# Optimization experiments

Measured on AMD Instinct MI355X. Metric: run time of the kernel, lower is better.

Reference implementation:

```python
import jax, jax.numpy as jnp
import numpy as np

B, D, H = 65536, 3, 256  # collocation batch, coord dim, hidden width


def setup_inputs() -> dict:
    key = jax.random.key(0)
    ks = jax.random.split(key, 8)

    def init(k, shape, fan_in):
        return jax.random.normal(k, shape, dtype=jnp.float32) * np.float32(1.0 / np.sqrt(fan_in))

    return {
        "x": jax.random.uniform(ks[0], (B, D), dtype=jnp.float32, minval=0.1, maxval=1.0),
        "W0": init(ks[1], (D, H), D), "b0": jnp.zeros((H,), jnp.float32),
        "W1": init(ks[2], (H, H), H), "b1": jnp.zeros((H,), jnp.float32),
        "W2": init(ks[3], (H, H), H), "b2": jnp.zeros((H,), jnp.float32),
        "W3": init(ks[4], (H, H), H), "b3": jnp.zeros((H,), jnp.float32),
        "Wout": init(ks[5], (H, 1), H), "bout": jnp.zeros((1,), jnp.float32),
    }


def reference(x, W0, b0, W1, b1, W2, b2, W3, b3, Wout, bout):
    # Scalar PINN network u(xi), xi: [D]
    def u_fn(xi):
        h = jnp.tanh(xi @ W0 + b0)
        h = jnp.tanh(h @ W1 + b1)
        h = jnp.tanh(h @ W2 + b2)
        h = jnp.tanh(h @ W3 + b3)
        return (h @ Wout + bout)[0]

    u = jax.vmap(u_fn)(x)                               # [B]
    # batch_gradient: du/dx_i for every coordinate axis (Cartesian: no adjustment)
    grads = jax.vmap(jax.grad(u_fn))(x)                 # [B, D]
    # batch_hessian diagonal: d^2u/dx_i^2 via forward-over-reverse
    hess_fn = jax.jacfwd(jax.grad(u_fn))                # [D, D] per sample
    hess_diag = jax.vmap(lambda xi: jnp.diagonal(hess_fn(xi)))(x)  # [B, D]
    # pack (u, grad, hessian-diagonal) as the PDE-residual ingredients
    return jnp.concatenate([u[:, None], grads, hess_diag], axis=1)  # [B, 1+D+D]
```

## Files before the change

### kernel.cpp

```cpp
#include <hip/hip_runtime.h>
#include <hip/hip_fp16.h>

#define HDIM 256
#define MS 16
#define LDAK 264
#define CSTRIDE (MS * LDAK * 2)

typedef _Float16 half8 __attribute__((ext_vector_type(8)));
typedef _Float16 half4 __attribute__((ext_vector_type(4)));
typedef _Float16 half2v __attribute__((ext_vector_type(2)));
typedef float f32x4 __attribute__((ext_vector_type(4)));

__device__ __forceinline__ float fast_tanh(float x) {
    float e = __expf(2.0f * x);
    return 1.0f - 2.0f * __builtin_amdgcn_rcpf(e + 1.0f);
}

__device__ __forceinline__ half4 cvt4(float a, float b, float c, float d) {
    half2v lo = __builtin_bit_cast(half2v, __builtin_amdgcn_cvt_pkrtz(a, b));
    half2v hi = __builtin_bit_cast(half2v, __builtin_amdgcn_cvt_pkrtz(c, d));
    half4 r; r[0] = lo[0]; r[1] = lo[1]; r[2] = hi[0]; r[3] = hi[1];
    return r;
}

__device__ __forceinline__ void barrier_lds() {
    asm volatile("s_waitcnt lgkmcnt(0)\n\ts_barrier" ::: "memory");
}

__global__ __launch_bounds__(256) void pack_weights(const float* __restrict__ W1,
                                                    const float* __restrict__ W2,
                                                    const float* __restrict__ W3,
                                                    _Float16* __restrict__ out) {
    int tid = blockIdx.x * 256 + threadIdx.x;
    int l = tid >> 13;
    int idx = tid & 8191;
    int kg = idx >> 8;
    int n = idx & 255;
    const float* W = (l == 0) ? W1 : (l == 1) ? W2 : W3;
    half8 v;
    #pragma unroll
    for (int j = 0; j < 8; ++j) v[j] = (_Float16)W[(kg * 8 + j) * 256 + n];
    *(half8*)(out + l * 65536 + kg * 2048 + n * 8) = v;
}

__global__ __launch_bounds__(512, 2)
void pinn_fused(const float* __restrict__ x,
                const float* __restrict__ W0,
                const float* __restrict__ b0,
                const float* __restrict__ b1,
                const float* __restrict__ b2,
                const float* __restrict__ b3,
                const float* __restrict__ Wout,
                const float* __restrict__ bout,
                const _Float16* __restrict__ Wp,
                float* __restrict__ out) {
    __shared__ __align__(16) _Float16 AbA[7 * MS][LDAK];
    __shared__ __align__(16) _Float16 AbB[7 * MS][LDAK];
    __shared__ float part[2][8 * 7 * MS];

    const int tid  = threadIdx.x;
    const int lane = tid & 63;
    const int wid  = tid >> 6;
    const int qd   = lane >> 4;
    const int n15  = lane & 15;
    const int base = blockIdx.x * (2 * MS);
    const int nw   = wid * 32 + n15;

    const int voff0 = (qd * 256 + nw) * 8;
    const int abase = (n15 * LDAK + qd * 8) * 2;
    const int sbase = (n15 * LDAK + wid * 32 + qd * 4) * 2;

    half8 wf[3][2];

#define PREF(J) do { \
    if ((J) < 48) { \
        const int g_ = (((J) >> 4) * 8) + ((J) & 7); \
        wf[(J) % 3][0] = *(const half8*)(Wp + g_ * 8192 + voff0); \
        wf[(J) % 3][1] = *(const half8*)(Wp + g_ * 8192 + voff0 + 128); \
    } \
} while (0)

#define KSTEP(ACC, AB, J) do { \
    const int s_ = (J) & 7; \
    PREF((J) + 2); \
    half8 af_[7]; \
    _Pragma("unroll") \
    for (int c_ = 0; c_ < 7; ++c_) \
        af_[c_] = *(const half8*)((const char*)AB + abase + c_ * CSTRIDE + s_ * 64); \
    _Pragma("unroll") \
    for (int c_ = 0; c_ < 7; ++c_) \
        _Pragma("unroll") \
        for (int t_ = 0; t_ < 2; ++t_) \
            ACC[c_][t_] = __builtin_amdgcn_mfma_f32_16x16x32_f16(wf[(J) % 3][t_], af_[c_], ACC[c_][t_], 0, 0, 0); \
} while (0)

#define ELEMW(ACC, AB, BB, T) do { \
    const int ncol_ = wid * 32 + (T) * 16 + qd * 4; \
    f32x4 bv_ = *(const f32x4*)((BB) + ncol_); \
    float tv_[4], gj_[3][4], sj_[3][4]; \
    _Pragma("unroll") \
    for (int r_ = 0; r_ < 4; ++r_) { \
        float zv_ = ACC[0][T][r_] + bv_[r_]; \
        tv_[r_] = fast_tanh(zv_); \
        float dd_ = 1.f - tv_[r_] * tv_[r_]; \
        float c2_ = -2.f * tv_[r_] * dd_; \
        _Pragma("unroll") \
        for (int i_ = 0; i_ < 3; ++i_) { \
            float zg_ = ACC[1 + i_][T][r_]; \
            float zs_ = ACC[4 + i_][T][r_]; \
            gj_[i_][r_] = dd_ * zg_; \
            sj_[i_][r_] = dd_ * zs_ + c2_ * zg_ * zg_; \
        } \
    } \
    char* sb_ = (char*)AB + sbase; \
    *(half4*)(sb_ + 0 * CSTRIDE + (T) * 32) = cvt4(tv_[0], tv_[1], tv_[2], tv_[3]); \
    _Pragma("unroll") \
    for (int i_ = 0; i_ < 3; ++i_) { \
        *(half4*)(sb_ + (1 + i_) * CSTRIDE + (T) * 32) = \
            cvt4(gj_[i_][0], gj_[i_][1], gj_[i_][2], gj_[i_][3]); \
        *(half4*)(sb_ + (4 + i_) * CSTRIDE + (T) * 32) = \
            cvt4(sj_[i_][0], sj_[i_][1], sj_[i_][2], sj_[i_][3]); \
    } \
} while (0)

#define L0G(AB, X0, X1, X2) do { \
    half8 h_[7]; \
    _Pragma("unroll") \
    for (int r_ = 0; r_ < 8; ++r_) { \
        const float w0_ = w0v[r_ >> 2][r_ & 3]; \
        const float w1_ = w1v[r_ >> 2][r_ & 3]; \
        const float w2_ = w2v[r_ >> 2][r_ & 3]; \
        float z_  = (X0) * w0_ + (X1) * w1_ + (X2) * w2_ + b0v[r_ >> 2][r_ & 3]; \
        float tv_ = fast_tanh(z_); \
        float dd_ = 1.f - tv_ * tv_; \
        float c2_ = -2.f * tv_ * dd_; \
        h_[0][r_] = (_Float16)tv_; \
        h_[1][r_] = (_Float16)(dd_ * w0_); \
        h_[2][r_] = (_Float16)(dd_ * w1_); \
        h_[3][r_] = (_Float16)(dd_ * w2_); \
        h_[4][r_] = (_Float16)(c2_ * w0_ * w0_); \
        h_[5][r_] = (_Float16)(c2_ * w1_ * w1_); \
        h_[6][r_] = (_Float16)(c2_ * w2_ * w2_); \
    } \
    _Pragma("unroll") \
    for (int c_ = 0; c_ < 7; ++c_) \
        *(half8*)&AB[c_ * MS + m0][n0] = h_[c_]; \
} while (0)

#define OUTG(ACC, G) do { \
    float p_[7] = {0.f, 0.f, 0.f, 0.f, 0.f, 0.f, 0.f}; \
    _Pragma("unroll") \
    for (int t_ = 0; t_ < 2; ++t_) { \
        const int ncol_ = wid * 32 + t_ * 16 + qd * 4; \
        f32x4 bv_ = *(const f32x4*)(b3 + ncol_); \
        f32x4 wv_ = *(const f32x4*)(Wout + ncol_); \
        _Pragma("unroll") \
        for (int r_ = 0; r_ < 4; ++r_) { \
            float zv_ = ACC[0][t_][r_] + bv_[r_]; \
            float tv_ = fast_tanh(zv_); \
            float dd_ = 1.f - tv_ * tv_; \
            float c2_ = -2.f * tv_ * dd_; \
            p_[0] += tv_ * wv_[r_]; \
            _Pragma("unroll") \
            for (int i_ = 0; i_ < 3; ++i_) { \
                float zg_ = ACC[1 + i_][t_][r_]; \
                float zs_ = ACC[4 + i_][t_][r_]; \
                p_[1 + i_] += (dd_ * zg_) * wv_[r_]; \
                p_[4 + i_] += (dd_ * zs_ + c2_ * zg_ * zg_) * wv_[r_]; \
            } \
        } \
    } \
    _Pragma("unroll") \
    for (int c_ = 0; c_ < 7; ++c_) { \
        p_[c_] += __shfl_xor(p_[c_], 16, 64); \
        p_[c_] += __shfl_xor(p_[c_], 32, 64); \
    } \
    if (lane < 16) { \
        _Pragma("unroll") \
        for (int c_ = 0; c_ < 7; ++c_) \
            part[G][(wid * 7 + c_) * MS + lane] = p_[c_]; \
    } \
} while (0)

#define ZACC(A_) do { \
    _Pragma("unroll") \
    for (int c_ = 0; c_ < 7; ++c_) \
        _Pragma("unroll") \
        for (int t_ = 0; t_ < 2; ++t_) A_[c_][t_] = (f32x4){0.f, 0.f, 0.f, 0.f}; \
} while (0)

    const int m0 = tid & 15;
    const int n0 = (tid >> 4) * 8;
    const float xa0 = x[(base + m0) * 3 + 0];
    const float xa1 = x[(base + m0) * 3 + 1];
    const float xa2 = x[(base + m0) * 3 + 2];
    const float xb0 = x[(base + MS + m0) * 3 + 0];
    const float xb1 = x[(base + MS + m0) * 3 + 1];
    const float xb2 = x[(base + MS + m0) * 3 + 2];

    PREF(0);
    PREF(1);

    f32x4 w0v[2], w1v[2], w2v[2], b0v[2];
    w0v[0] = *(const f32x4*)(W0 + n0);            w0v[1] = *(const f32x4*)(W0 + n0 + 4);
    w1v[0] = *(const f32x4*)(W0 + HDIM + n0);     w1v[1] = *(const f32x4*)(W0 + HDIM + n0 + 4);
    w2v[0] = *(const f32x4*)(W0 + 2 * HDIM + n0); w2v[1] = *(const f32x4*)(W0 + 2 * HDIM + n0 + 4);
    b0v[0] = *(const f32x4*)(b0 + n0);            b0v[1] = *(const f32x4*)(b0 + n0 + 4);

    f32x4 accA[7][2], accB[7][2];

    L0G(AbA, xa0, xa1, xa2);
    barrier_lds();

    ZACC(accA);
    KSTEP(accA, AbA, 0);
    KSTEP(accA, AbA, 1);
    L0G(AbB, xb0, xb1, xb2);
    KSTEP(accA, AbA, 2); KSTEP(accA, AbA, 3); KSTEP(accA, AbA, 4);
    KSTEP(accA, AbA, 5); KSTEP(accA, AbA, 6); KSTEP(accA, AbA, 7);
    barrier_lds();

    ZACC(accB);
    KSTEP(accB, AbB, 8);
    ELEMW(accA, AbA, b1, 0);
    KSTEP(accB, AbB, 9); KSTEP(accB, AbB, 10); KSTEP(accB, AbB, 11);
    ELEMW(accA, AbA, b1, 1);
    KSTEP(accB, AbB, 12); KSTEP(accB, AbB, 13); KSTEP(accB, AbB, 14); KSTEP(accB, AbB, 15);
    barrier_lds();

    ZACC(accA);
    KSTEP(accA, AbA, 16);
    ELEMW(accB, AbB, b1, 0);
    KSTEP(accA, AbA, 17); KSTEP(accA, AbA, 18); KSTEP(accA, AbA, 19);
    ELEMW(accB, AbB, b1, 1);
    KSTEP(accA, AbA, 20); KSTEP(accA, AbA, 21); KSTEP(accA, AbA, 22); KSTEP(accA, AbA, 23);
    barrier_lds();

    ZACC(accB);
    KSTEP(accB, AbB, 24);
    ELEMW(accA, AbA, b2, 0);
    KSTEP(accB, AbB, 25); KSTEP(accB, AbB, 26); KSTEP(accB, AbB, 27);
    ELEMW(accA, AbA, b2, 1);
    KSTEP(accB, AbB, 28); KSTEP(accB, AbB, 29); KSTEP(accB, AbB, 30); KSTEP(accB, AbB, 31);
    barrier_lds();

    ZACC(accA);
    KSTEP(accA, AbA, 32);
    ELEMW(accB, AbB, b2, 0);
    KSTEP(accA, AbA, 33); KSTEP(accA, AbA, 34); KSTEP(accA, AbA, 35);
    ELEMW(accB, AbB, b2, 1);
    KSTEP(accA, AbA, 36); KSTEP(accA, AbA, 37); KSTEP(accA, AbA, 38); KSTEP(accA, AbA, 39);
    barrier_lds();

    ZACC(accB);
    KSTEP(accB, AbB, 40); KSTEP(accB, AbB, 41);
    OUTG(accA, 0);
    KSTEP(accB, AbB, 42); KSTEP(accB, AbB, 43); KSTEP(accB, AbB, 44);
    KSTEP(accB, AbB, 45); KSTEP(accB, AbB, 46); KSTEP(accB, AbB, 47);
    OUTG(accB, 1);
    barrier_lds();

    if ((tid & 255) < 112) {
        const int g = tid >> 8;
        const int c = (tid & 255) >> 4;
        const int m = tid & 15;
        float v = 0.f;
        #pragma unroll
        for (int w = 0; w < 8; ++w) v += part[g][(w * 7 + c) * MS + m];
        if (c == 0) v += bout[0];
        out[(base + g * MS + m) * 7 + c] = v;
    }

#undef PREF
#undef KSTEP
#undef ELEMW
#undef L0G
#undef OUTG
#undef ZACC
}

extern "C" void kernel_launch(void* const* d_in, const int* in_sizes, int n_in,
                              void* d_out, int out_size, void* d_ws, size_t ws_size,
                              hipStream_t stream) {
    const float* xp   = (const float*)d_in[0];
    const float* W0   = (const float*)d_in[1];
    const float* b0   = (const float*)d_in[2];
    const float* W1   = (const float*)d_in[3];
    const float* b1   = (const float*)d_in[4];
    const float* W2   = (const float*)d_in[5];
    const float* b2   = (const float*)d_in[6];
    const float* W3   = (const float*)d_in[7];
    const float* b3   = (const float*)d_in[8];
    const float* Wout = (const float*)d_in[9];
    const float* bout = (const float*)d_in[10];
    _Float16* Wp = (_Float16*)d_ws;

    pack_weights<<<96, 256, 0, stream>>>(W1, W2, W3, Wp);
    pinn_fused<<<65536 / (2 * MS), 512, 0, stream>>>(xp, W0, b0, b1, b2, b3, Wout, bout,
                                                     Wp, (float*)d_out);
}
```

Baseline: 263.1 us.

## Split block into two wave groups ping-ponging GEMM and elementwise phases

The 8 waves are split into two groups of 4, each owning one 16-sample tile. Each wave now covers 64 output columns, so accumulators grow to 7x4 and weight fragments are loaded at 4 per step. The groups alternate, so one runs MFMA k-loops while the other runs tanh and derivative elementwise work, with s_setprio raised around the MFMA bursts. This aims to overlap VALU and matrix work across waves and halve weight loads per sample, at the cost of higher register pressure from the larger accumulators, which risks lower occupancy or spills.

```diff
diff --git a/kernel.cpp b/kernel.cpp
--- a/kernel.cpp
+++ b/kernel.cpp
@@ -54,117 +54,158 @@
                 const float* __restrict__ bout,
                 const _Float16* __restrict__ Wp,
                 float* __restrict__ out) {
-    __shared__ __align__(16) _Float16 AbA[7 * MS][LDAK];
-    __shared__ __align__(16) _Float16 AbB[7 * MS][LDAK];
-    __shared__ float part[2][8 * 7 * MS];
+    __shared__ __align__(16) _Float16 Abuf[2][7 * MS][LDAK];
+    __shared__ float part[2][4 * 7 * MS];
 
     const int tid  = threadIdx.x;
     const int lane = tid & 63;
     const int wid  = tid >> 6;
+    const int grp  = wid >> 2;
+    const int wq   = wid & 3;
     const int qd   = lane >> 4;
     const int n15  = lane & 15;
-    const int base = blockIdx.x * (2 * MS);
-    const int nw   = wid * 32 + n15;
+    const int base = blockIdx.x * (2 * MS) + grp * MS;
+    const int nw   = wq * 64 + n15;
 
     const int voff0 = (qd * 256 + nw) * 8;
+    const char* Ab  = (const char*)&Abuf[grp][0][0];
     const int abase = (n15 * LDAK + qd * 8) * 2;
-    const int sbase = (n15 * LDAK + wid * 32 + qd * 4) * 2;
-
-    half8 wf[3][2];
-
-#define PREF(J) do { \
-    if ((J) < 48) { \
-        const int g_ = (((J) >> 4) * 8) + ((J) & 7); \
-        wf[(J) % 3][0] = *(const half8*)(Wp + g_ * 8192 + voff0); \
-        wf[(J) % 3][1] = *(const half8*)(Wp + g_ * 8192 + voff0 + 128); \
-    } \
-} while (0)
-
-#define KSTEP(ACC, AB, J) do { \
-    const int s_ = (J) & 7; \
-    PREF((J) + 2); \
-    half8 af_[7]; \
+    char* Sb        = (char*)&Abuf[grp][0][0];
+    const int sbase = (n15 * LDAK + wq * 64 + qd * 4) * 2;
+
+    half8 wf[3][4];
+
+#define PREFW(L, S, BUF) do { \
+    _Pragma("unroll") \
+    for (int t_ = 0; t_ < 4; ++t_) \
+        wf[BUF][t_] = *(const half8*)(Wp + ((L) * 8 + (S)) * 8192 + voff0 + t_ * 128); \
+} while (0)
+
+#define PREF2(L) do { PREFW(L, 0, 0); PREFW(L, 1, 1); } while (0)
+
+#define LDAF(AF, S) do { \
     _Pragma("unroll") \
     for (int c_ = 0; c_ < 7; ++c_) \
-        af_[c_] = *(const half8*)((const char*)AB + abase + c_ * CSTRIDE + s_ * 64); \
+        AF[c_] = *(const half8*)(Ab + abase + c_ * CSTRIDE + (S) * 64); \
+} while (0)
+
+#define MMS(ACC, AF, WB) do { \
+    __builtin_amdgcn_s_setprio(1); \
     _Pragma("unroll") \
     for (int c_ = 0; c_ < 7; ++c_) \
         _Pragma("unroll") \
-        for (int t_ = 0; t_ < 2; ++t_) \
-            ACC[c_][t_] = __builtin_amdgcn_mfma_f32_16x16x32_f16(wf[(J) % 3][t_], af_[c_], ACC[c_][t_], 0, 0, 0); \
-} while (0)
-
-#define ELEMW(ACC, AB, BB, T) do { \
-    const int ncol_ = wid * 32 + (T) * 16 + qd * 4; \
-    f32x4 bv_ = *(const f32x4*)((BB) + ncol_); \
-    float tv_[4], gj_[3][4], sj_[3][4]; \
-    _Pragma("unroll") \
-    for (int r_ = 0; r_ < 4; ++r_) { \
-        float zv_ = ACC[0][T][r_] + bv_[r_]; \
-        tv_[r_] = fast_tanh(zv_); \
-        float dd_ = 1.f - tv_[r_] * tv_[r_]; \
-        float c2_ = -2.f * tv_[r_] * dd_; \
+        for (int t_ = 0; t_ < 4; ++t_) \
+            ACC[c_][t_] = __builtin_amdgcn_mfma_f32_16x16x32_f16(wf[WB][t_], AF[c_], ACC[c_][t_], 0, 0, 0); \
+    __builtin_amdgcn_s_setprio(0); \
+} while (0)
+
+#define KLOOP(ACC, L) do { \
+    half8 afX[7], afY[7]; \
+    LDAF(afX, 0); LDAF(afY, 1); \
+    PREFW(L, 2, 2); MMS(ACC, afX, 0); LDAF(afX, 2); \
+    PREFW(L, 3, 0); MMS(ACC, afY, 1); LDAF(afY, 3); \
+    PREFW(L, 4, 1); MMS(ACC, afX, 2); LDAF(afX, 4); \
+    PREFW(L, 5, 2); MMS(ACC, afY, 0); LDAF(afY, 5); \
+    PREFW(L, 6, 0); MMS(ACC, afX, 1); LDAF(afX, 6); \
+    PREFW(L, 7, 1); MMS(ACC, afY, 2); LDAF(afY, 7); \
+    MMS(ACC, afX, 0); \
+    MMS(ACC, afY, 1); \
+} while (0)
+
+#define ZACC(A_) do { \
+    _Pragma("unroll") \
+    for (int c_ = 0; c_ < 7; ++c_) \
+        _Pragma("unroll") \
+        for (int t_ = 0; t_ < 4; ++t_) A_[c_][t_] = (f32x4){0.f, 0.f, 0.f, 0.f}; \
+} while (0)
+
+#define L0G() do { \
+    const int m_  = tid & 15; \
+    const int nb_ = ((tid & 255) >> 4) * 16; \
+    const float x0_ = x[(base + m_) * 3 + 0]; \
+    const float x1_ = x[(base + m_) * 3 + 1]; \
+    const float x2_ = x[(base + m_) * 3 + 2]; \
+    _Pragma("unroll") \
+    for (int ch_ = 0; ch_ < 2; ++ch_) { \
+        const int n0_ = nb_ + ch_ * 8; \
+        f32x4 w0v_[2], w1v_[2], w2v_[2], bv_[2]; \
+        w0v_[0] = *(const f32x4*)(W0 + n0_);            w0v_[1] = *(const f32x4*)(W0 + n0_ + 4); \
+        w1v_[0] = *(const f32x4*)(W0 + HDIM + n0_);     w1v_[1] = *(const f32x4*)(W0 + HDIM + n0_ + 4); \
+        w2v_[0] = *(const f32x4*)(W0 + 2 * HDIM + n0_); w2v_[1] = *(const f32x4*)(W0 + 2 * HDIM + n0_ + 4); \
+        bv_[0]  = *(const f32x4*)(b0 + n0_);            bv_[1]  = *(const f32x4*)(b0 + n0_ + 4); \
+        half8 h_[7]; \
+        _Pragma("unroll") \
+        for (int r_ = 0; r_ < 8; ++r_) { \
+            const float w0_ = w0v_[r_ >> 2][r_ & 3]; \
+            const float w1_ = w1v_[r_ >> 2][r_ & 3]; \
+            const float w2_ = w2v_[r_ >> 2][r_ & 3]; \
+            float z_  = x0_ * w0_ + x1_ * w1_ + x2_ * w2_ + bv_[r_ >> 2][r_ & 3]; \
+            float tv_ = fast_tanh(z_); \
+            float dd_ = 1.f - tv_ * tv_; \
+            float c2_ = -2.f * tv_ * dd_; \
+            h_[0][r_] = (_Float16)tv_; \
+            h_[1][r_] = (_Float16)(dd_ * w0_); \
+            h_[2][r_] = (_Float16)(dd_ * w1_); \
+            h_[3][r_] = (_Float16)(dd_ * w2_); \
+            h_[4][r_] = (_Float16)(c2_ * w0_ * w0_); \
+            h_[5][r_] = (_Float16)(c2_ * w1_ * w1_); \
+            h_[6][r_] = (_Float16)(c2_ * w2_ * w2_); \
+        } \
+        _Pragma("unroll") \
+        for (int c_ = 0; c_ < 7; ++c_) \
+            *(half8*)&Abuf[grp][c_ * MS + m_][n0_] = h_[c_]; \
+    } \
+} while (0)
+
+#define ELEMW(ACC, BB) do { \
+    _Pragma("unroll") \
+    for (int tt_ = 0; tt_ < 4; ++tt_) { \
+        const int ncol_ = wq * 64 + tt_ * 16 + qd * 4; \
+        f32x4 bv_ = *(const f32x4*)((BB) + ncol_); \
+        float tv_[4], gj_[3][4], sj_[3][4]; \
+        _Pragma("unroll") \
+        for (int r_ = 0; r_ < 4; ++r_) { \
+            float zv_ = ACC[0][tt_][r_] + bv_[r_]; \
+            tv_[r_] = fast_tanh(zv_); \
+            float dd_ = 1.f - tv_[r_] * tv_[r_]; \
+            float c2_ = -2.f * tv_[r_] * dd_; \
+            _Pragma("unroll") \
+            for (int i_ = 0; i_ < 3; ++i_) { \
+                float zg_ = ACC[1 + i_][tt_][r_]; \
+                float zs_ = ACC[4 + i_][tt_][r_]; \
+                gj_[i_][r_] = dd_ * zg_; \
+                sj_[i_][r_] = dd_ * zs_ + c2_ * zg_ * zg_; \
+            } \
+        } \
+        *(half4*)(Sb + sbase + 0 * CSTRIDE + tt_ * 32) = cvt4(tv_[0], tv_[1], tv_[2], tv_[3]); \
         _Pragma("unroll") \
         for (int i_ = 0; i_ < 3; ++i_) { \
-            float zg_ = ACC[1 + i_][T][r_]; \
-            float zs_ = ACC[4 + i_][T][r_]; \
-            gj_[i_][r_] = dd_ * zg_; \
-            sj_[i_][r_] = dd_ * zs_ + c2_ * zg_ * zg_; \
-        } \
-    } \
-    char* sb_ = (char*)AB + sbase; \
-    *(half4*)(sb_ + 0 * CSTRIDE + (T) * 32) = cvt4(tv_[0], tv_[1], tv_[2], tv_[3]); \
-    _Pragma("unroll") \
-    for (int i_ = 0; i_ < 3; ++i_) { \
-        *(half4*)(sb_ + (1 + i_) * CSTRIDE + (T) * 32) = \
-            cvt4(gj_[i_][0], gj_[i_][1], gj_[i_][2], gj_[i_][3]); \
-        *(half4*)(sb_ + (4 + i_) * CSTRIDE + (T) * 32) = \
-            cvt4(sj_[i_][0], sj_[i_][1], sj_[i_][2], sj_[i_][3]); \
-    } \
-} while (0)
-
-#define L0G(AB, X0, X1, X2) do { \
-    half8 h_[7]; \
-    _Pragma("unroll") \
-    for (int r_ = 0; r_ < 8; ++r_) { \
-        const float w0_ = w0v[r_ >> 2][r_ & 3]; \
-        const float w1_ = w1v[r_ >> 2][r_ & 3]; \
-        const float w2_ = w2v[r_ >> 2][r_ & 3]; \
-        float z_  = (X0) * w0_ + (X1) * w1_ + (X2) * w2_ + b0v[r_ >> 2][r_ & 3]; \
-        float tv_ = fast_tanh(z_); \
-        float dd_ = 1.f - tv_ * tv_; \
-        float c2_ = -2.f * tv_ * dd_; \
-        h_[0][r_] = (_Float16)tv_; \
-        h_[1][r_] = (_Float16)(dd_ * w0_); \
-        h_[2][r_] = (_Float16)(dd_ * w1_); \
-        h_[3][r_] = (_Float16)(dd_ * w2_); \
-        h_[4][r_] = (_Float16)(c2_ * w0_ * w0_); \
-        h_[5][r_] = (_Float16)(c2_ * w1_ * w1_); \
-        h_[6][r_] = (_Float16)(c2_ * w2_ * w2_); \
-    } \
-    _Pragma("unroll") \
-    for (int c_ = 0; c_ < 7; ++c_) \
-        *(half8*)&AB[c_ * MS + m0][n0] = h_[c_]; \
+            *(half4*)(Sb + sbase + (1 + i_) * CSTRIDE + tt_ * 32) = \
+                cvt4(gj_[i_][0], gj_[i_][1], gj_[i_][2], gj_[i_][3]); \
+            *(half4*)(Sb + sbase + (4 + i_) * CSTRIDE + tt_ * 32) = \
+                cvt4(sj_[i_][0], sj_[i_][1], sj_[i_][2], sj_[i_][3]); \
+        } \
+    } \
 } while (0)
 
 #define OUTG(ACC, G) do { \
     float p_[7] = {0.f, 0.f, 0.f, 0.f, 0.f, 0.f, 0.f}; \
     _Pragma("unroll") \
-    for (int t_ = 0; t_ < 2; ++t_) { \
-        const int ncol_ = wid * 32 + t_ * 16 + qd * 4; \
+    for (int tt_ = 0; tt_ < 4; ++tt_) { \
+        const int ncol_ = wq * 64 + tt_ * 16 + qd * 4; \
         f32x4 bv_ = *(const f32x4*)(b3 + ncol_); \
         f32x4 wv_ = *(const f32x4*)(Wout + ncol_); \
         _Pragma("unroll") \
         for (int r_ = 0; r_ < 4; ++r_) { \
-            float zv_ = ACC[0][t_][r_] + bv_[r_]; \
+            float zv_ = ACC[0][tt_][r_] + bv_[r_]; \
             float tv_ = fast_tanh(zv_); \
             float dd_ = 1.f - tv_ * tv_; \
             float c2_ = -2.f * tv_ * dd_; \
             p_[0] += tv_ * wv_[r_]; \
             _Pragma("unroll") \
             for (int i_ = 0; i_ < 3; ++i_) { \
-                float zg_ = ACC[1 + i_][t_][r_]; \
-                float zs_ = ACC[4 + i_][t_][r_]; \
+                float zg_ = ACC[1 + i_][tt_][r_]; \
+                float zs_ = ACC[4 + i_][tt_][r_]; \
                 p_[1 + i_] += (dd_ * zg_) * wv_[r_]; \
                 p_[4 + i_] += (dd_ * zs_ + c2_ * zg_ * zg_) * wv_[r_]; \
             } \
@@ -178,105 +219,59 @@
     if (lane < 16) { \
         _Pragma("unroll") \
         for (int c_ = 0; c_ < 7; ++c_) \
-            part[G][(wid * 7 + c_) * MS + lane] = p_[c_]; \
-    } \
-} while (0)
-
-#define ZACC(A_) do { \
-    _Pragma("unroll") \
-    for (int c_ = 0; c_ < 7; ++c_) \
-        _Pragma("unroll") \
-        for (int t_ = 0; t_ < 2; ++t_) A_[c_][t_] = (f32x4){0.f, 0.f, 0.f, 0.f}; \
-} while (0)
-
-    const int m0 = tid & 15;
-    const int n0 = (tid >> 4) * 8;
-    const float xa0 = x[(base + m0) * 3 + 0];
-    const float xa1 = x[(base + m0) * 3 + 1];
-    const float xa2 = x[(base + m0) * 3 + 2];
-    const float xb0 = x[(base + MS + m0) * 3 + 0];
-    const float xb1 = x[(base + MS + m0) * 3 + 1];
-    const float xb2 = x[(base + MS + m0) * 3 + 2];
-
-    PREF(0);
-    PREF(1);
-
-    f32x4 w0v[2], w1v[2], w2v[2], b0v[2];
-    w0v[0] = *(const f32x4*)(W0 + n0);            w0v[1] = *(const f32x4*)(W0 + n0 + 4);
-    w1v[0] = *(const f32x4*)(W0 + HDIM + n0);     w1v[1] = *(const f32x4*)(W0 + HDIM + n0 + 4);
-    w2v[0] = *(const f32x4*)(W0 + 2 * HDIM + n0); w2v[1] = *(const f32x4*)(W0 + 2 * HDIM + n0 + 4);
-    b0v[0] = *(const f32x4*)(b0 + n0);            b0v[1] = *(const f32x4*)(b0 + n0 + 4);
-
-    f32x4 accA[7][2], accB[7][2];
-
-    L0G(AbA, xa0, xa1, xa2);
-    barrier_lds();
-
-    ZACC(accA);
-    KSTEP(accA, AbA, 0);
-    KSTEP(accA, AbA, 1);
-    L0G(AbB, xb0, xb1, xb2);
-    KSTEP(accA, AbA, 2); KSTEP(accA, AbA, 3); KSTEP(accA, AbA, 4);
-    KSTEP(accA, AbA, 5); KSTEP(accA, AbA, 6); KSTEP(accA, AbA, 7);
-    barrier_lds();
-
-    ZACC(accB);
-    KSTEP(accB, AbB, 8);
-    ELEMW(accA, AbA, b1, 0);
-    KSTEP(accB, AbB, 9); KSTEP(accB, AbB, 10); KSTEP(accB, AbB, 11);
-    ELEMW(accA, AbA, b1, 1);
-    KSTEP(accB, AbB, 12); KSTEP(accB, AbB, 13); KSTEP(accB, AbB, 14); KSTEP(accB, AbB, 15);
-    barrier_lds();
-
-    ZACC(accA);
-    KSTEP(accA, AbA, 16);
-    ELEMW(accB, AbB, b1, 0);
-    KSTEP(accA, AbA, 17); KSTEP(accA, AbA, 18); KSTEP(accA, AbA, 19);
-    ELEMW(accB, AbB, b1, 1);
-    KSTEP(accA, AbA, 20); KSTEP(accA, AbA, 21); KSTEP(accA, AbA, 22); KSTEP(accA, AbA, 23);
-    barrier_lds();
-
-    ZACC(accB);
-    KSTEP(accB, AbB, 24);
-    ELEMW(accA, AbA, b2, 0);
-    KSTEP(accB, AbB, 25); KSTEP(accB, AbB, 26); KSTEP(accB, AbB, 27);
-    ELEMW(accA, AbA, b2, 1);
-    KSTEP(accB, AbB, 28); KSTEP(accB, AbB, 29); KSTEP(accB, AbB, 30); KSTEP(accB, AbB, 31);
-    barrier_lds();
-
-    ZACC(accA);
-    KSTEP(accA, AbA, 32);
-    ELEMW(accB, AbB, b2, 0);
-    KSTEP(accA, AbA, 33); KSTEP(accA, AbA, 34); KSTEP(accA, AbA, 35);
-    ELEMW(accB, AbB, b2, 1);
-    KSTEP(accA, AbA, 36); KSTEP(accA, AbA, 37); KSTEP(accA, AbA, 38); KSTEP(accA, AbA, 39);
-    barrier_lds();
-
-    ZACC(accB);
-    KSTEP(accB, AbB, 40); KSTEP(accB, AbB, 41);
-    OUTG(accA, 0);
-    KSTEP(accB, AbB, 42); KSTEP(accB, AbB, 43); KSTEP(accB, AbB, 44);
-    KSTEP(accB, AbB, 45); KSTEP(accB, AbB, 46); KSTEP(accB, AbB, 47);
-    OUTG(accB, 1);
+            part[G][(wq * 7 + c_) * MS + lane] = p_[c_]; \
+    } \
+} while (0)
+
+    f32x4 acc[7][4];
+    PREF2(0);
+
+    if (grp == 0) { L0G(); }
+    barrier_lds();
+
+    if (grp == 0) { ZACC(acc); KLOOP(acc, 0); }
+    else          { L0G(); }
+    barrier_lds();
+
+    if (grp == 0) { ELEMW(acc, b1); PREF2(1); }
+    else          { ZACC(acc); KLOOP(acc, 0); }
+    barrier_lds();
+
+    if (grp == 0) { ZACC(acc); KLOOP(acc, 1); }
+    else          { ELEMW(acc, b1); PREF2(1); }
+    barrier_lds();
+
+    if (grp == 0) { ELEMW(acc, b2); PREF2(2); }
+    else          { ZACC(acc); KLOOP(acc, 1); }
+    barrier_lds();
+
+    if (grp == 0) { ZACC(acc); KLOOP(acc, 2); }
+    else          { ELEMW(acc, b2); PREF2(2); }
+    barrier_lds();
+
+    if (grp == 0) { OUTG(acc, 0); }
+    else          { ZACC(acc); KLOOP(acc, 2); OUTG(acc, 1); }
     barrier_lds();
 
     if ((tid & 255) < 112) {
         const int g = tid >> 8;
         const int c = (tid & 255) >> 4;
         const int m = tid & 15;
-        float v = 0.f;
-        #pragma unroll
-        for (int w = 0; w < 8; ++w) v += part[g][(w * 7 + c) * MS + m];
+        float v = part[g][(0 * 7 + c) * MS + m] + part[g][(1 * 7 + c) * MS + m] +
+                  part[g][(2 * 7 + c) * MS + m] + part[g][(3 * 7 + c) * MS + m];
         if (c == 0) v += bout[0];
-        out[(base + g * MS + m) * 7 + c] = v;
+        out[(blockIdx.x * (2 * MS) + g * MS + m) * 7 + c] = v;
     }
 
-#undef PREF
-#undef KSTEP
+#undef PREFW
+#undef PREF2
+#undef LDAF
+#undef MMS
+#undef KLOOP
+#undef ZACC
+#undef L0G
 #undef ELEMW
-#undef L0G
 #undef OUTG
-#undef ZACC
 }
 
 extern "C" void kernel_launch(void* const* d_in, const int* in_sizes, int n_in,
```

Result: no change. 258.8 us (-1.6%).
